# Optimization experiments

Measured on AMD Instinct MI355X. Metric: run time of the kernel, lower is better.

Reference implementation:

```python
import jax, jax.numpy as jnp
import numpy as np
from jax.scipy.special import logsumexp

N_LABELS = 64
BOS_INDEX = 0
B, S = 32, 512


def setup_inputs() -> dict:
    key = jax.random.key(0)
    k1, k2, k3 = jax.random.split(key, 3)
    emits = jax.random.normal(k1, (B, S, N_LABELS * N_LABELS), dtype=jnp.float32)
    targets = jax.random.randint(k2, (B, S + 1), 0, N_LABELS, dtype=jnp.int64)
    # mask: valid-prefix mask from random lengths in [2, S]
    lengths = jax.random.randint(k3, (B,), 2, S + 1)
    mask = (jnp.arange(S)[None, :] < lengths[:, None])
    return {"emits": emits, "targets": targets, "mask": mask}


def reference(emits, targets, mask):
    # emits: [B, S, L*L], targets: [B, S+1], mask: [B, S]; order=2 CRF NLL loss
    L = N_LABELS
    b, s, _ = emits.shape
    em = jnp.transpose(emits, (1, 0, 2))          # [S, B, L*L]
    tg = targets.T                                 # [S+1, B]
    mk = mask.T                                    # [S, B]

    em4 = em.reshape(s, b, L, L)                   # [S, B, prev, next]
    log_alpha0 = em4[0, :, BOS_INDEX, :]           # [B, L]

    def step(log_alpha, inp):
        e_i, m_i = inp                             # [B, L, L], [B]
        scores = log_alpha[:, :, None] + e_i       # [B, prev, next]
        new = logsumexp(scores, axis=1)            # [B, L]
        log_alpha = jnp.where(m_i[:, None], new, log_alpha)
        return log_alpha, None

    log_alpha, _ = jax.lax.scan(step, log_alpha0, (em4[1:], mk[1:]))
    log_z = logsumexp(log_alpha, axis=1).sum()

    # gold path score: pair index = prev_tag * L + next_tag
    idx = tg[:-1] * L + tg[1:]                     # [S, B]
    gold = jnp.take_along_axis(em, idx[:, :, None], axis=-1)[..., 0]  # [S, B]
    score = jnp.where(mk, gold, 0.0).sum()

    total_token = mk.sum().astype(emits.dtype)
    loss = (log_z - score) / total_token
    return loss
```

## Files before the change

kernel.cpp:

```cpp
#include <hip/hip_runtime.h>
#include <math.h>


constexpr int S_LEN   = 512;
constexpr int NB      = 32;
constexpr int NL      = 64;
constexpr int LL      = 4096;
constexpr int CL      = 16;
constexpr int NCH     = 32;
constexpr int NCHUNKS = NB * NCH;
constexpr int XSTR    = 68;

#define LN2F 0.69314718055994531f
#define PREF 4.6588830833596715f

typedef _Float16 h4 __attribute__((ext_vector_type(4)));
typedef float    f4 __attribute__((ext_vector_type(4)));
union U4 { unsigned u[2]; h4 v; };

__device__ __forceinline__ float bl(float v, int sl) {
  return __int_as_float(__builtin_amdgcn_readlane(__float_as_int(v), sl));
}
__device__ __forceinline__ unsigned pk2(float a, float b) {
  auto r = __builtin_amdgcn_cvt_pkrtz(a, b);
  return __builtin_bit_cast(unsigned, r);
}
__device__ __forceinline__ float expw(float x) {
  return __expf(x - PREF);
}

__global__ __launch_bounds__(128, 2) void crf_chunk(
    const float* __restrict__ emits,
    const int*   __restrict__ targets,
    const int*   __restrict__ mask,
    _Float16*    __restrict__ matP,
    float*       __restrict__ wsf)
{
  __shared__ _Float16 xch[64 * XSTR];
  __shared__ float    xLacc;

  const int ci   = blockIdx.x;
  const int b    = ci >> 5;
  const int cc   = ci & 31;
  const int tid  = threadIdx.x;
  const int wave = tid >> 6;
  const int lane = tid & 63;
  const int c    = lane & 15;
  const int h    = lane >> 4;
  const float* __restrict__ eb = emits + (size_t)b * (S_LEN * LL);

  int len;
  {
    const int* mb = mask + b * S_LEN;
    int cnt = 0;
    #pragma unroll
    for (int i = 0; i < 8; ++i) cnt += (mb[i * 64 + lane] != 0);
    #pragma unroll
    for (int off = 32; off; off >>= 1) cnt += __shfl_xor(cnt, off);
    len = cnt;
  }

  if (wave == 0) {
    float g = 0.f;
    const int s = 16 * cc + (lane & 15);
    if (lane < 16 && s < len) {
      const int* tb = targets + b * (S_LEN + 1);
      g = eb[(size_t)s * LL + tb[s] * NL + tb[s + 1]];
    }
    #pragma unroll
    for (int off = 32; off; off >>= 1) g += __shfl_xor(g, off);
    if (lane == 0) wsf[NCHUNKS + ci] = g;
  }

  const int s0 = 16 * cc + 1;
  const int n  = min(len - s0, CL);
  if (n < 1) return;

  const int n0    = min(n, 8);
  const int nw    = wave ? (n - n0) : n0;
  const int sbase = wave ? (s0 + 8) : s0;

  h4 bf[4][4];
  #pragma unroll
  for (int K = 0; K < 4; ++K)
    #pragma unroll
    for (int J = 0; J < 4; ++J) {
      h4 v;
      #pragma unroll
      for (int i = 0; i < 4; ++i)
        v[i] = (_Float16)((K == J && (4 * h + i) == c) ? 1.0f : 0.0f);
      bf[K][J] = v;
    }

  float Lacc = 0.f;
  f4 LB0[4][4], LB1[4][4];
  h4 af[4][4];

#define LOADE(LB, S)                                                         \
  do { const float* ep = eb + (size_t)(S) * LL;                              \
    _Pragma("unroll") for (int I = 0; I < 4; ++I) {                          \
      const float* rp = ep + (16 * I + c) * 64 + 4 * h;                      \
      _Pragma("unroll") for (int K = 0; K < 4; ++K)                          \
        LB[I][K] = *reinterpret_cast<const f4*>(rp + 16 * K);                \
    } } while (0)

#define BUILDAF(LB)                                                          \
  do { _Pragma("unroll") for (int I = 0; I < 4; ++I)                         \
    _Pragma("unroll") for (int K = 0; K < 4; ++K) {                          \
      U4 x;                                                                  \
      x.u[0] = pk2(expw(LB[I][K][0]), expw(LB[I][K][1]));                    \
      x.u[1] = pk2(expw(LB[I][K][2]), expw(LB[I][K][3]));                    \
      af[I][K] = x.v;                                                        \
    } } while (0)

#define STEPM(LBC, M)                                                        \
  do { if ((M) <= nw) {                                                      \
    BUILDAF(LBC);                                                            \
    if ((M) + 2 <= nw) LOADE(LBC, sbase + nw - 2 - (M));                     \
    const bool rn = ((M) == nw) || (((M) & 7) == 0);                         \
    float mh = 0.f;                                                          \
    { f4 dh[4][2];                                                           \
      _Pragma("unroll") for (int I = 0; I < 4; ++I)                          \
        _Pragma("unroll") for (int J = 0; J < 2; ++J) {                      \
          f4 d = {0.f, 0.f, 0.f, 0.f};                                       \
          _Pragma("unroll") for (int K = 0; K < 4; ++K)                      \
            d = __builtin_amdgcn_mfma_f32_16x16x16f16(af[I][K], bf[K][J], d, 0, 0, 0); \
          dh[I][J] = d;                                                      \
        }                                                                    \
      if (rn) { _Pragma("unroll") for (int I = 0; I < 4; ++I)                \
        _Pragma("unroll") for (int J = 0; J < 2; ++J)                        \
          _Pragma("unroll") for (int u = 0; u < 4; ++u)                      \
            mh = fmaxf(mh, dh[I][J][u]); }                                   \
      _Pragma("unroll") for (int K = 0; K < 4; ++K)                          \
        _Pragma("unroll") for (int J = 0; J < 2; ++J) {                      \
          U4 y;                                                              \
          y.u[0] = pk2(dh[K][J][0], dh[K][J][1]);                            \
          y.u[1] = pk2(dh[K][J][2], dh[K][J][3]);                            \
          bf[K][J] = y.v;                                                    \
        } }                                                                  \
    { f4 dh[4][2];                                                           \
      _Pragma("unroll") for (int I = 0; I < 4; ++I)                          \
        _Pragma("unroll") for (int J = 0; J < 2; ++J) {                      \
          f4 d = {0.f, 0.f, 0.f, 0.f};                                       \
          _Pragma("unroll") for (int K = 0; K < 4; ++K)                      \
            d = __builtin_amdgcn_mfma_f32_16x16x16f16(af[I][K], bf[K][J + 2], d, 0, 0, 0); \
          dh[I][J] = d;                                                      \
        }                                                                    \
      if (rn) { _Pragma("unroll") for (int I = 0; I < 4; ++I)                \
        _Pragma("unroll") for (int J = 0; J < 2; ++J)                        \
          _Pragma("unroll") for (int u = 0; u < 4; ++u)                      \
            mh = fmaxf(mh, dh[I][J][u]); }                                   \
      _Pragma("unroll") for (int K = 0; K < 4; ++K)                          \
        _Pragma("unroll") for (int J = 0; J < 2; ++J) {                      \
          U4 y;                                                              \
          y.u[0] = pk2(dh[K][J][0], dh[K][J][1]);                            \
          y.u[1] = pk2(dh[K][J][2], dh[K][J][3]);                            \
          bf[K][J + 2] = y.v;                                                \
        } }                                                                  \
    Lacc += PREF;                                                            \
    if (rn) {                                                                \
      _Pragma("unroll") for (int off = 32; off; off >>= 1)                   \
        mh = fmaxf(mh, __shfl_xor(mh, off));                                 \
      const int E = (__float_as_int(mh) >> 23) & 0xFF;                       \
      const _Float16 hs = (_Float16)__int_as_float((254 - E) << 23);         \
      const h4 hv = {hs, hs, hs, hs};                                        \
      _Pragma("unroll") for (int K = 0; K < 4; ++K)                          \
        _Pragma("unroll") for (int J = 0; J < 4; ++J) bf[K][J] *= hv;        \
      Lacc += (float)(E - 127) * LN2F;                                       \
    }                                                                        \
  } } while (0)

  if (nw >= 1) {
    LOADE(LB0, sbase + nw - 1);
    if (nw > 1) LOADE(LB1, sbase + nw - 2);
    for (int m = 1; m <= nw; m += 2) {
      STEPM(LB0, m);
      STEPM(LB1, m + 1);
    }
  }

  if (wave == 0) {
    #pragma unroll
    for (int K = 0; K < 4; ++K)
      #pragma unroll
      for (int J = 0; J < 4; ++J)
        *reinterpret_cast<h4*>(&xch[(16 * J + c) * XSTR + 16 * K + 4 * h]) = bf[K][J];
    if (lane == 0) xLacc = Lacc;
  }
  __syncthreads();

  if (wave == 1) {
    h4 afl[4][4];
    #pragma unroll
    for (int I = 0; I < 4; ++I)
      #pragma unroll
      for (int K = 0; K < 4; ++K)
        afl[I][K] = *reinterpret_cast<const h4*>(
            &xch[(16 * I + c) * XSTR + 16 * K + 4 * h]);

    float mh = 0.f;
    #pragma unroll
    for (int half = 0; half < 2; ++half) {
      f4 dh[4][2];
      #pragma unroll
      for (int I = 0; I < 4; ++I)
        #pragma unroll
        for (int J = 0; J < 2; ++J) {
          f4 d = {0.f, 0.f, 0.f, 0.f};
          #pragma unroll
          for (int K = 0; K < 4; ++K)
            d = __builtin_amdgcn_mfma_f32_16x16x16f16(
                afl[I][K], bf[K][J + 2 * half], d, 0, 0, 0);
          dh[I][J] = d;
        }
      #pragma unroll
      for (int I = 0; I < 4; ++I)
        #pragma unroll
        for (int J = 0; J < 2; ++J)
          #pragma unroll
          for (int u = 0; u < 4; ++u) mh = fmaxf(mh, dh[I][J][u]);
      #pragma unroll
      for (int K = 0; K < 4; ++K)
        #pragma unroll
        for (int J = 0; J < 2; ++J) {
          U4 y;
          y.u[0] = pk2(dh[K][J][0], dh[K][J][1]);
          y.u[1] = pk2(dh[K][J][2], dh[K][J][3]);
          bf[K][J + 2 * half] = y.v;
        }
    }
    #pragma unroll
    for (int off = 32; off; off >>= 1) mh = fmaxf(mh, __shfl_xor(mh, off));
    const int E = (__float_as_int(mh) >> 23) & 0xFF;
    const _Float16 hs = (_Float16)__int_as_float((254 - E) << 23);
    const h4 hv = {hs, hs, hs, hs};
    #pragma unroll
    for (int K = 0; K < 4; ++K)
      #pragma unroll
      for (int J = 0; J < 4; ++J) bf[K][J] *= hv;
    const float Ltot = Lacc + xLacc + (float)(E - 127) * LN2F;

    _Float16* mp = matP + (size_t)ci * 4096;
    #pragma unroll
    for (int I = 0; I < 4; ++I)
      #pragma unroll
      for (int J = 0; J < 4; ++J)
        #pragma unroll
        for (int i = 0; i < 4; ++i)
          mp[(I * 4 + J) * 256 + i * 64 + lane] = bf[I][J][i];
    if (lane == 0) wsf[ci] = Ltot;
  }
}

__global__ __launch_bounds__(64) void crf_fold(
    const float* __restrict__ emits,
    const int*   __restrict__ mask,
    const _Float16* __restrict__ matP,
    const float* __restrict__ wsf,
    float*       __restrict__ wso,
    int*         __restrict__ done,
    float*       __restrict__ out)
{
  const int b = blockIdx.x, lane = threadIdx.x;
  const int c = lane & 15, h = lane >> 4;
  const float* __restrict__ eb = emits + (size_t)b * (S_LEN * LL);

  int len;
  {
    const int* mb = mask + b * S_LEN;
    int cnt = 0;
    #pragma unroll
    for (int i = 0; i < 8; ++i) cnt += (mb[i * 64 + lane] != 0);
    #pragma unroll
    for (int off = 32; off; off >>= 1) cnt += __shfl_xor(cnt, off);
    len = cnt;
  }
  const int nact = (len + 14) >> 4;

  const bool on = (c == 0);
  const h4 HZ = {(_Float16)0, (_Float16)0, (_Float16)0, (_Float16)0};

  float la[16];
  #pragma unroll
  for (int K = 0; K < 4; ++K)
    #pragma unroll
    for (int i = 0; i < 4; ++i) la[K * 4 + i] = eb[16 * K + 4 * h + i];
  float mm = la[0];
  #pragma unroll
  for (int i = 1; i < 16; ++i) mm = fmaxf(mm, la[i]);
  const float m0 = fmaxf(fmaxf(bl(mm, 0), bl(mm, 16)), fmaxf(bl(mm, 32), bl(mm, 48)));
  float Lacc = m0;
  h4 bv[4];
  #pragma unroll
  for (int K = 0; K < 4; ++K) {
    U4 y;
    y.u[0] = pk2(__expf(la[4 * K] - m0), __expf(la[4 * K + 1] - m0));
    y.u[1] = pk2(__expf(la[4 * K + 2] - m0), __expf(la[4 * K + 3] - m0));
    bv[K] = on ? y.v : HZ;
  }

  h4 A0[4][4], A1[4][4], A2[4][4], A3[4][4];

#define LOADA(AF, CH)                                                        \
  do { const _Float16* mp = matP + (size_t)(b * NCH + (CH)) * 4096;          \
    _Pragma("unroll") for (int I = 0; I < 4; ++I)                            \
      _Pragma("unroll") for (int K = 0; K < 4; ++K)                          \
        AF[I][K] = *reinterpret_cast<const h4*>(                             \
            mp + (I * 4 + K) * 256 + (c & 3) * 64 + 16 * (c >> 2) + 4 * h);  \
  } while (0)

#define FOLD(AF, CH)                                                         \
  do { f4 dv[4];                                                             \
    _Pragma("unroll") for (int I = 0; I < 4; ++I) {                          \
      f4 d = {0.f, 0.f, 0.f, 0.f};                                           \
      _Pragma("unroll") for (int K = 0; K < 4; ++K)                          \
        d = __builtin_amdgcn_mfma_f32_16x16x16f16(AF[I][K], bv[K], d, 0, 0, 0); \
      dv[I] = d;                                                             \
    }                                                                        \
    float mx = dv[0][0];                                                     \
    _Pragma("unroll") for (int I = 0; I < 4; ++I)                            \
      _Pragma("unroll") for (int u = 0; u < 4; ++u) mx = fmaxf(mx, dv[I][u]); \
    float gm;                                                                \
    if (((CH) & 3) == 3) {                                                   \
      gm = fmaxf(fmaxf(bl(mx, 0), bl(mx, 16)),                               \
                 fmaxf(bl(mx, 32), bl(mx, 48)));                             \
    } else {                                                                 \
      gm = bl(mx, 0);                                                        \
    }                                                                        \
    const int E = (__float_as_int(gm) >> 23) & 0xFF;                         \
    const float scale = __int_as_float((254 - E) << 23);                     \
    Lacc += (float)(E - 127) * LN2F + wsf[b * NCH + (CH)];                   \
    _Pragma("unroll") for (int I = 0; I < 4; ++I) {                          \
      U4 y;                                                                  \
      y.u[0] = pk2(dv[I][0] * scale, dv[I][1] * scale);                      \
      y.u[1] = pk2(dv[I][2] * scale, dv[I][3] * scale);                      \
      bv[I] = on ? y.v : HZ;                                                 \
    } } while (0)

#define FSTEP(AF, APre, CH)                                                  \
  do { if ((CH) < nact) {                                                    \
    if ((CH) + 3 < nact) LOADA(APre, (CH) + 3);                              \
    FOLD(AF, (CH));                                                          \
  } } while (0)

  LOADA(A0, 0);
  if (1 < nact) LOADA(A1, 1);
  if (2 < nact) LOADA(A2, 2);
  for (int ch = 0; ch < nact; ch += 4) {
    FSTEP(A0, A3, ch);
    FSTEP(A1, A0, ch + 1);
    FSTEP(A2, A1, ch + 2);
    FSTEP(A3, A2, ch + 3);
  }

  float qs = 0.f;
  #pragma unroll
  for (int K = 0; K < 4; ++K)
    #pragma unroll
    for (int i = 0; i < 4; ++i) qs += (float)bv[K][i];
  const float q0 = (bl(qs, 0) + bl(qs, 16)) + (bl(qs, 32) + bl(qs, 48));
  if (lane == 0) {
    wso[b]      = Lacc + __logf(q0);
    wso[32 + b] = (float)len;
  }

  __threadfence();
  int isLast = 0;
  if (lane == 0) isLast = (atomicAdd(done, 1) == NB - 1);
  isLast = __shfl(isLast, 0);
  if (isLast) {
    __threadfence();
    const float* gold = wsf + NCHUNKS;
    float gs = 0.f;
    #pragma unroll
    for (int i = 0; i < NCHUNKS / 64; ++i) gs += gold[i * 64 + lane];
    float lz = (lane < NB) ? wso[lane] : 0.f;
    float ln = (lane < NB) ? wso[32 + lane] : 0.f;
    #pragma unroll
    for (int off = 32; off; off >>= 1) {
      gs += __shfl_xor(gs, off);
      lz += __shfl_xor(lz, off);
      ln += __shfl_xor(ln, off);
    }
    if (lane == 0) out[0] = (lz - gs) / ln;
  }
}

extern "C" void kernel_launch(void* const* d_in, const int* in_sizes, int n_in,
                              void* d_out, int out_size, void* d_ws, size_t ws_size,
                              hipStream_t stream) {
  const float* emits   = (const float*)d_in[0];
  const int*   targets = (const int*)d_in[1];
  const int*   mask    = (const int*)d_in[2];
  float* out = (float*)d_out;

  _Float16* matP = (_Float16*)d_ws;
  float*    wsf  = (float*)((char*)d_ws + (size_t)NCHUNKS * 4096 * 2);
  float*    wso  = wsf + 2 * NCHUNKS;
  int*      done = (int*)(wso + 64);

  hipMemsetAsync(done, 0, sizeof(int), stream);
  hipLaunchKernelGGL(crf_chunk, dim3(NCHUNKS), dim3(128), 0, stream,
                     emits, targets, mask, matP, wsf);
  hipLaunchKernelGGL(crf_fold, dim3(NB), dim3(64), 0, stream,
                     emits, mask, matP, wsf, wso, done, out);
}
```

Before: 75.76 us.

## Parallelize chunk-matrix fold across four waves with tree reduction, drop memset

The fold kernel now launches four waves per batch. Each wave multiplies up to eight consecutive chunk transfer matrices into a partial product through MFMA matrix-matrix products with per-step exponent rescaling, and stores the result in shared memory. Wave 0 then applies the four partial products to the initial vector in sequence. This shortens the serial dependency chain of matrix-vector folds, in exchange for full matrix-matrix work that costs more MFMAs and fp16 rescaling in the partial products. The done-counter memset is also replaced by a reset inside the chunk kernel, which removes one stream operation.

Result: faster. 65.24 us (-13.9%).

```diff
diff --git a/kernel.cpp b/kernel.cpp
--- a/kernel.cpp
+++ b/kernel.cpp
@@ -34,7 +34,8 @@
     const int*   __restrict__ targets,
     const int*   __restrict__ mask,
     _Float16*    __restrict__ matP,
-    float*       __restrict__ wsf)
+    float*       __restrict__ wsf,
+    int*         __restrict__ done)
 {
   __shared__ _Float16 xch[64 * XSTR];
   __shared__ float    xLacc;
@@ -48,6 +49,8 @@
   const int c    = lane & 15;
   const int h    = lane >> 4;
   const float* __restrict__ eb = emits + (size_t)b * (S_LEN * LL);
+
+  if (ci == 0 && tid == 0) *done = 0;
 
   int len;
   {
@@ -252,7 +255,7 @@
   }
 }
 
-__global__ __launch_bounds__(64) void crf_fold(
+__global__ __launch_bounds__(256) void crf_fold(
     const float* __restrict__ emits,
     const int*   __restrict__ mask,
     const _Float16* __restrict__ matP,
@@ -261,8 +264,15 @@
     int*         __restrict__ done,
     float*       __restrict__ out)
 {
-  const int b = blockIdx.x, lane = threadIdx.x;
-  const int c = lane & 15, h = lane >> 4;
+  __shared__ _Float16 xq[4][64 * XSTR];
+  __shared__ float    xL[4];
+
+  const int b    = blockIdx.x;
+  const int tid  = threadIdx.x;
+  const int wave = tid >> 6;
+  const int lane = tid & 63;
+  const int c    = lane & 15;
+  const int h    = lane >> 4;
   const float* __restrict__ eb = emits + (size_t)b * (S_LEN * LL);
 
   int len;
@@ -276,6 +286,119 @@
     len = cnt;
   }
   const int nact = (len + 14) >> 4;
+
+  const int j0 = 8 * wave;
+  const int j1 = min(nact, j0 + 8);
+
+  h4 bf[4][4];
+  #pragma unroll
+  for (int K = 0; K < 4; ++K)
+    #pragma unroll
+    for (int J = 0; J < 4; ++J) {
+      h4 v;
+      #pragma unroll
+      for (int i = 0; i < 4; ++i)
+        v[i] = (_Float16)((K == J && (4 * h + i) == c) ? 1.0f : 0.0f);
+      bf[K][J] = v;
+    }
+  float LaccQ = 0.f;
+
+  h4 A0[4][4], A1[4][4], A2[4][4];
+
+#define LOADA(AF, CH)                                                        \
+  do { const _Float16* mp = matP + (size_t)(b * NCH + (CH)) * 4096;          \
+    _Pragma("unroll") for (int I = 0; I < 4; ++I)                            \
+      _Pragma("unroll") for (int K = 0; K < 4; ++K)                          \
+        AF[I][K] = *reinterpret_cast<const h4*>(                             \
+            mp + (I * 4 + K) * 256 + (c & 3) * 64 + 16 * (c >> 2) + 4 * h);  \
+  } while (0)
+
+#define MPROD(ACUR, RNFULL, JJ)                                              \
+  do {                                                                       \
+    float mh = 0.f;                                                          \
+    { f4 dh[4][2];                                                           \
+      _Pragma("unroll") for (int I = 0; I < 4; ++I)                          \
+        _Pragma("unroll") for (int J = 0; J < 2; ++J) {                      \
+          f4 d = {0.f, 0.f, 0.f, 0.f};                                       \
+          _Pragma("unroll") for (int K = 0; K < 4; ++K)                      \
+            d = __builtin_amdgcn_mfma_f32_16x16x16f16(ACUR[I][K], bf[K][J], d, 0, 0, 0); \
+          dh[I][J] = d;                                                      \
+        }                                                                    \
+      _Pragma("unroll") for (int I = 0; I < 4; ++I)                          \
+        _Pragma("unroll") for (int J = 0; J < 2; ++J)                        \
+          _Pragma("unroll") for (int u = 0; u < 4; ++u)                      \
+            mh = fmaxf(mh, dh[I][J][u]);                                     \
+      _Pragma("unroll") for (int K = 0; K < 4; ++K)                          \
+        _Pragma("unroll") for (int J = 0; J < 2; ++J) {                      \
+          U4 y;                                                              \
+          y.u[0] = pk2(dh[K][J][0], dh[K][J][1]);                            \
+          y.u[1] = pk2(dh[K][J][2], dh[K][J][3]);                            \
+          bf[K][J] = y.v;                                                    \
+        } }                                                                  \
+    { f4 dh[4][2];                                                           \
+      _Pragma("unroll") for (int I = 0; I < 4; ++I)                          \
+        _Pragma("unroll") for (int J = 0; J < 2; ++J) {                      \
+          f4 d = {0.f, 0.f, 0.f, 0.f};                                       \
+          _Pragma("unroll") for (int K = 0; K < 4; ++K)                      \
+            d = __builtin_amdgcn_mfma_f32_16x16x16f16(ACUR[I][K], bf[K][J + 2], d, 0, 0, 0); \
+          dh[I][J] = d;                                                      \
+        }                                                                    \
+      _Pragma("unroll") for (int I = 0; I < 4; ++I)                          \
+        _Pragma("unroll") for (int J = 0; J < 2; ++J)                        \
+          _Pragma("unroll") for (int u = 0; u < 4; ++u)                      \
+            mh = fmaxf(mh, dh[I][J][u]);                                     \
+      _Pragma("unroll") for (int K = 0; K < 4; ++K)                          \
+        _Pragma("unroll") for (int J = 0; J < 2; ++J) {                      \
+          U4 y;                                                              \
+          y.u[0] = pk2(dh[K][J][0], dh[K][J][1]);                            \
+          y.u[1] = pk2(dh[K][J][2], dh[K][J][3]);                            \
+          bf[K][J + 2] = y.v;                                                \
+        } }                                                                  \
+    float gm;                                                                \
+    if (RNFULL) {                                                            \
+      _Pragma("unroll") for (int off = 32; off; off >>= 1)                   \
+        mh = fmaxf(mh, __shfl_xor(mh, off));                                 \
+      gm = mh;                                                               \
+    } else {                                                                 \
+      gm = bl(mh, 0);                                                        \
+    }                                                                        \
+    const int E = (__float_as_int(gm) >> 23) & 0xFF;                         \
+    const _Float16 hs = (_Float16)__int_as_float((254 - E) << 23);           \
+    const h4 hv = {hs, hs, hs, hs};                                          \
+    _Pragma("unroll") for (int K = 0; K < 4; ++K)                            \
+      _Pragma("unroll") for (int J = 0; J < 4; ++J) bf[K][J] *= hv;          \
+    LaccQ += (float)(E - 127) * LN2F + wsf[b * NCH + (JJ)];                  \
+  } while (0)
+
+#define QSTEP(ACUR, APRE, KO)                                                \
+  do { const int jj = j0 + (KO);                                             \
+    if (jj < j1) {                                                           \
+      if (jj + 2 < j1) LOADA(APRE, jj + 2);                                  \
+      MPROD(ACUR, ((((KO) & 1) == 1) || (jj == j1 - 1)), jj);                \
+    } } while (0)
+
+  if (j0 < j1) {
+    LOADA(A0, j0);
+    if (j0 + 1 < j1) LOADA(A1, j0 + 1);
+    QSTEP(A0, A2, 0);
+    QSTEP(A1, A0, 1);
+    QSTEP(A2, A1, 2);
+    QSTEP(A0, A2, 3);
+    QSTEP(A1, A0, 4);
+    QSTEP(A2, A1, 5);
+    QSTEP(A0, A2, 6);
+    QSTEP(A1, A0, 7);
+  }
+
+  #pragma unroll
+  for (int K = 0; K < 4; ++K)
+    #pragma unroll
+    for (int J = 0; J < 4; ++J)
+      *reinterpret_cast<h4*>(&xq[wave][(16 * J + c) * XSTR + 16 * K + 4 * h]) = bf[K][J];
+  if (lane == 0) xL[wave] = LaccQ;
+  __syncthreads();
+
+  if (wave != 0) return;
 
   const bool on = (c == 0);
   const h4 HZ = {(_Float16)0, (_Float16)0, (_Float16)0, (_Float16)0};
@@ -299,37 +422,34 @@
     bv[K] = on ? y.v : HZ;
   }
 
-  h4 A0[4][4], A1[4][4], A2[4][4], A3[4][4];
-
-#define LOADA(AF, CH)                                                        \
-  do { const _Float16* mp = matP + (size_t)(b * NCH + (CH)) * 4096;          \
+#define APPLYQ(W, LASTF)                                                     \
+  do {                                                                       \
+    h4 afl[4][4];                                                            \
     _Pragma("unroll") for (int I = 0; I < 4; ++I)                            \
       _Pragma("unroll") for (int K = 0; K < 4; ++K)                          \
-        AF[I][K] = *reinterpret_cast<const h4*>(                             \
-            mp + (I * 4 + K) * 256 + (c & 3) * 64 + 16 * (c >> 2) + 4 * h);  \
-  } while (0)
-
-#define FOLD(AF, CH)                                                         \
-  do { f4 dv[4];                                                             \
+        afl[I][K] = *reinterpret_cast<const h4*>(                            \
+            &xq[W][(16 * I + c) * XSTR + 16 * K + 4 * h]);                   \
+    f4 dv[4];                                                                \
     _Pragma("unroll") for (int I = 0; I < 4; ++I) {                          \
       f4 d = {0.f, 0.f, 0.f, 0.f};                                           \
       _Pragma("unroll") for (int K = 0; K < 4; ++K)                          \
-        d = __builtin_amdgcn_mfma_f32_16x16x16f16(AF[I][K], bv[K], d, 0, 0, 0); \
+        d = __builtin_amdgcn_mfma_f32_16x16x16f16(afl[I][K], bv[K], d, 0, 0, 0); \
       dv[I] = d;                                                             \
     }                                                                        \
     float mx = dv[0][0];                                                     \
     _Pragma("unroll") for (int I = 0; I < 4; ++I)                            \
       _Pragma("unroll") for (int u = 0; u < 4; ++u) mx = fmaxf(mx, dv[I][u]); \
     float gm;                                                                \
-    if (((CH) & 3) == 3) {                                                   \
-      gm = fmaxf(fmaxf(bl(mx, 0), bl(mx, 16)),                               \
-                 fmaxf(bl(mx, 32), bl(mx, 48)));                             \
+    if (LASTF) {                                                             \
+      _Pragma("unroll") for (int off = 32; off; off >>= 1)                   \
+        mx = fmaxf(mx, __shfl_xor(mx, off));                                 \
+      gm = mx;                                                               \
     } else {                                                                 \
       gm = bl(mx, 0);                                                        \
     }                                                                        \
     const int E = (__float_as_int(gm) >> 23) & 0xFF;                         \
     const float scale = __int_as_float((254 - E) << 23);                     \
-    Lacc += (float)(E - 127) * LN2F + wsf[b * NCH + (CH)];                   \
+    Lacc += (float)(E - 127) * LN2F + xL[W];                                 \
     _Pragma("unroll") for (int I = 0; I < 4; ++I) {                          \
       U4 y;                                                                  \
       y.u[0] = pk2(dv[I][0] * scale, dv[I][1] * scale);                      \
@@ -337,21 +457,10 @@
       bv[I] = on ? y.v : HZ;                                                 \
     } } while (0)
 
-#define FSTEP(AF, APre, CH)                                                  \
-  do { if ((CH) < nact) {                                                    \
-    if ((CH) + 3 < nact) LOADA(APre, (CH) + 3);                              \
-    FOLD(AF, (CH));                                                          \
-  } } while (0)
-
-  LOADA(A0, 0);
-  if (1 < nact) LOADA(A1, 1);
-  if (2 < nact) LOADA(A2, 2);
-  for (int ch = 0; ch < nact; ch += 4) {
-    FSTEP(A0, A3, ch);
-    FSTEP(A1, A0, ch + 1);
-    FSTEP(A2, A1, ch + 2);
-    FSTEP(A3, A2, ch + 3);
-  }
+  APPLYQ(0, false);
+  APPLYQ(1, false);
+  APPLYQ(2, false);
+  APPLYQ(3, true);
 
   float qs = 0.f;
   #pragma unroll
@@ -399,9 +508,8 @@
   float*    wso  = wsf + 2 * NCHUNKS;
   int*      done = (int*)(wso + 64);
 
-  hipMemsetAsync(done, 0, sizeof(int), stream);
   hipLaunchKernelGGL(crf_chunk, dim3(NCHUNKS), dim3(128), 0, stream,
-                     emits, targets, mask, matP, wsf);
-  hipLaunchKernelGGL(crf_fold, dim3(NB), dim3(64), 0, stream,
+                     emits, targets, mask, matP, wsf, done);
+  hipLaunchKernelGGL(crf_fold, dim3(NB), dim3(256), 0, stream,
                      emits, mask, matP, wsf, wso, done, out);
 }
```
